# Optimization experiments

Hardware: AMD Instinct MI355X
Metric: run time of the kernel (lower is better)

The kernel has to match this reference:

```python
import jax, jax.numpy as jnp
import numpy as np

B, S, D_IN, D_OUT, RANK = 4, 2048, 4096, 4096, 16
SCALING = 32.0 / RANK  # alpha / rank
MASK_DENSITY = 0.01


def setup_inputs() -> dict:
    key = jax.random.key(0)
    ks = jax.random.split(key, 7)
    x = jax.random.normal(ks[0], (B, S, D_IN), dtype=jnp.float32)
    W = jax.random.normal(ks[1], (D_OUT, D_IN), dtype=jnp.float32) / np.sqrt(D_IN)
    b = jax.random.normal(ks[2], (D_OUT,), dtype=jnp.float32) * 0.01
    lora_A = jax.random.normal(ks[3], (RANK, D_IN), dtype=jnp.float32) / np.sqrt(D_IN)
    lora_B = jax.random.normal(ks[4], (D_OUT, RANK), dtype=jnp.float32) * 0.01
    delta = jax.random.normal(ks[5], (D_OUT, D_IN), dtype=jnp.float32) * 0.01
    mask = jax.random.bernoulli(ks[6], MASK_DENSITY, (D_OUT, D_IN))
    return {"x": x, "W": W, "b": b, "lora_A": lora_A, "lora_B": lora_B,
            "delta": delta, "mask": mask}


def reference(x, W, b, lora_A, lora_B, delta, mask):
    # frozen linear: [B,S,D_in] @ [D_in,D_out] + b
    out = jnp.einsum("bsd,od->bso", x, W) + b
    # LoRA branch: (x @ A^T) @ B^T * scaling
    out = out + jnp.einsum("bsr,or->bso", jnp.einsum("bsd,rd->bsr", x, lora_A), lora_B) * SCALING
    # sparse delta branch: F.linear(x, delta * mask)
    masked_delta = delta * mask.astype(delta.dtype)
    out = out + jnp.einsum("bsd,od->bso", x, masked_delta)
    return out
```

## Files before the change

kernel.cpp:

```cpp
#include <hip/hip_runtime.h>
#include <hip/hip_bf16.h>

typedef __hip_bfloat16 bf16;
typedef __attribute__((ext_vector_type(8))) short bf16x8;
typedef __attribute__((ext_vector_type(4))) float f32x4;
typedef __attribute__((ext_vector_type(4))) int int4v;

#define AS1 __attribute__((address_space(1)))
#define AS3 __attribute__((address_space(3)))

#define MDIM 8192
#define NDIM 4096
#define KDIM 4096
#define SCALING 2.0f

__global__ __launch_bounds__(256) void fold_weff(
    const float* __restrict__ W, const float* __restrict__ lA,
    const float* __restrict__ lB, const float* __restrict__ delta,
    const int* __restrict__ mask, bf16* __restrict__ Weff)
{
    int idx = blockIdx.x * 256 + threadIdx.x;
    int o   = idx >> 9;
    int d0  = (idx & 511) << 3;
    size_t base = (size_t)o * KDIM + d0;

    float Bo[16];
#pragma unroll
    for (int r = 0; r < 16; ++r) Bo[r] = lB[o * 16 + r];

    f32x4 wa = *(const f32x4*)(W + base);
    f32x4 wb = *(const f32x4*)(W + base + 4);
    f32x4 da = *(const f32x4*)(delta + base);
    f32x4 db = *(const f32x4*)(delta + base + 4);

    int mk[8];
    *(int4v*)(mk)     = *(const int4v*)(mask + base);
    *(int4v*)(mk + 4) = *(const int4v*)(mask + base + 4);

    float lor[8] = {0.f, 0.f, 0.f, 0.f, 0.f, 0.f, 0.f, 0.f};
#pragma unroll
    for (int r = 0; r < 16; ++r) {
        f32x4 aa = *(const f32x4*)(lA + (size_t)r * KDIM + d0);
        f32x4 ab = *(const f32x4*)(lA + (size_t)r * KDIM + d0 + 4);
#pragma unroll
        for (int e = 0; e < 4; ++e) {
            lor[e]     += Bo[r] * aa[e];
            lor[e + 4] += Bo[r] * ab[e];
        }
    }

    int4v ov4;
    bf16* ov = (bf16*)&ov4;
#pragma unroll
    for (int e = 0; e < 8; ++e) {
        float w = (e < 4) ? wa[e] : wb[e - 4];
        float d = (e < 4) ? da[e] : db[e - 4];
        float a = w + SCALING * lor[e];
        if (mk[e]) a += d;
        ov[e] = __float2bfloat16(a);
    }
    *(int4v*)(Weff + base) = ov4;
}

__global__ __launch_bounds__(256) void convert_x(
    const float* __restrict__ X, bf16* __restrict__ Xb)
{
    size_t i = ((size_t)blockIdx.x * 256 + threadIdx.x) * 8;
    f32x4 a = *(const f32x4*)(X + i);
    f32x4 b = *(const f32x4*)(X + i + 4);
    int4v ov4;
    bf16* ov = (bf16*)&ov4;
#pragma unroll
    for (int e = 0; e < 4; ++e) {
        ov[e]     = __float2bfloat16(a[e]);
        ov[e + 4] = __float2bfloat16(b[e]);
    }
    *(int4v*)(Xb + i) = ov4;
}

__global__ __launch_bounds__(256, 4) void gemm_bf16(
    const bf16* __restrict__ X, const bf16* __restrict__ Wt,
    const float* __restrict__ bias, float* __restrict__ out)
{
    __shared__ bf16 As[128 * 64];
    __shared__ bf16 Bs[128 * 64];

    const int tid  = threadIdx.x;
    const int lane = tid & 63;
    const int wave = tid >> 6;
    const int wm   = wave & 1;
    const int wn   = wave >> 1;
    const int quad = lane >> 4;
    const int l16  = lane & 15;

    const int bn = blockIdx.x * 128;
    const int bm = blockIdx.y * 128;
    const int cwave = tid & ~63;

    f32x4 acc[4][4];
#pragma unroll
    for (int i = 0; i < 4; ++i)
#pragma unroll
        for (int j = 0; j < 4; ++j)
            acc[i][j] = (f32x4){0.f, 0.f, 0.f, 0.f};

    for (int kt = 0; kt < KDIM / 64; ++kt) {
        const int k0 = kt * 64;
        if (kt) __syncthreads();
#pragma unroll
        for (int j = 0; j < 4; ++j) {
            const int c  = j * 256 + tid;
            const int m  = c >> 3;
            const int kc = (c & 7) ^ (m & 7);
            const int cb = j * 256 + cwave;
            __builtin_amdgcn_global_load_lds(
                (const AS1 void*)(X + (size_t)(bm + m) * KDIM + k0 + kc * 8),
                (AS3 void*)(As + cb * 8), 16, 0, 0);
            __builtin_amdgcn_global_load_lds(
                (const AS1 void*)(Wt + (size_t)(bn + m) * KDIM + k0 + kc * 8),
                (AS3 void*)(Bs + cb * 8), 16, 0, 0);
        }
        __syncthreads();

#pragma unroll
        for (int ks = 0; ks < 2; ++ks) {
            bf16x8 af[4], bfr[4];
#pragma unroll
            for (int i = 0; i < 4; ++i) {
                const int m   = wm * 64 + i * 16 + l16;
                const int kca = (ks * 4 + quad) ^ (m & 7);
                af[i] = *(const bf16x8*)(As + m * 64 + kca * 8);
                const int n   = wn * 64 + i * 16 + l16;
                const int kcb = (ks * 4 + quad) ^ (n & 7);
                bfr[i] = *(const bf16x8*)(Bs + n * 64 + kcb * 8);
            }
#pragma unroll
            for (int i = 0; i < 4; ++i)
#pragma unroll
                for (int j = 0; j < 4; ++j)
                    acc[i][j] = __builtin_amdgcn_mfma_f32_16x16x32_bf16(
                        af[i], bfr[j], acc[i][j], 0, 0, 0);
        }
    }

    float bv[4];
#pragma unroll
    for (int j = 0; j < 4; ++j)
        bv[j] = bias[bn + wn * 64 + j * 16 + l16];

#pragma unroll
    for (int i = 0; i < 4; ++i) {
        const int mg = bm + wm * 64 + i * 16 + quad * 4;
#pragma unroll
        for (int j = 0; j < 4; ++j) {
            const int ng = bn + wn * 64 + j * 16 + l16;
#pragma unroll
            for (int r = 0; r < 4; ++r)
                out[(size_t)(mg + r) * NDIM + ng] = acc[i][j][r] + bv[j];
        }
    }
}

__global__ __launch_bounds__(256, 3) void gemm_f32(
    const float* __restrict__ X, const bf16* __restrict__ Wt,
    const float* __restrict__ bias, float* __restrict__ out)
{
    __shared__ float Asf[128 * 64];
    __shared__ bf16  Bs[128 * 64];

    const int tid  = threadIdx.x;
    const int lane = tid & 63;
    const int wave = tid >> 6;
    const int wm   = wave & 1;
    const int wn   = wave >> 1;
    const int quad = lane >> 4;
    const int l16  = lane & 15;

    const int bn = blockIdx.x * 128;
    const int bm = blockIdx.y * 128;
    const int cwave = tid & ~63;

    f32x4 acc[4][4];
#pragma unroll
    for (int i = 0; i < 4; ++i)
#pragma unroll
        for (int j = 0; j < 4; ++j)
            acc[i][j] = (f32x4){0.f, 0.f, 0.f, 0.f};

    for (int kt = 0; kt < KDIM / 64; ++kt) {
        const int k0 = kt * 64;
        if (kt) __syncthreads();
#pragma unroll
        for (int j = 0; j < 8; ++j) {
            const int c  = j * 256 + tid;
            const int m  = c >> 4;
            const int kc = (c & 15) ^ (m & 15);
            const int cb = j * 256 + cwave;
            __builtin_amdgcn_global_load_lds(
                (const AS1 void*)(X + (size_t)(bm + m) * KDIM + k0 + kc * 4),
                (AS3 void*)(Asf + cb * 4), 16, 0, 0);
        }
#pragma unroll
        for (int j = 0; j < 4; ++j) {
            const int c  = j * 256 + tid;
            const int m  = c >> 3;
            const int kc = (c & 7) ^ (m & 7);
            const int cb = j * 256 + cwave;
            __builtin_amdgcn_global_load_lds(
                (const AS1 void*)(Wt + (size_t)(bn + m) * KDIM + k0 + kc * 8),
                (AS3 void*)(Bs + cb * 8), 16, 0, 0);
        }
        __syncthreads();

#pragma unroll
        for (int ks = 0; ks < 2; ++ks) {
            bf16x8 af[4], bfr[4];
#pragma unroll
            for (int i = 0; i < 4; ++i) {
                const int m  = wm * 64 + i * 16 + l16;
                const int k2 = (ks * 4 + quad) * 2;
                f32x4 lo = *(const f32x4*)(Asf + m * 64 + ((k2     ^ (m & 15)) * 4));
                f32x4 hi = *(const f32x4*)(Asf + m * 64 + (((k2+1) ^ (m & 15)) * 4));
                bf16 tmp[8];
#pragma unroll
                for (int e = 0; e < 4; ++e) {
                    tmp[e]     = __float2bfloat16(lo[e]);
                    tmp[e + 4] = __float2bfloat16(hi[e]);
                }
                af[i] = *(const bf16x8*)tmp;

                const int n   = wn * 64 + i * 16 + l16;
                const int kcb = (ks * 4 + quad) ^ (n & 7);
                bfr[i] = *(const bf16x8*)(Bs + n * 64 + kcb * 8);
            }
#pragma unroll
            for (int i = 0; i < 4; ++i)
#pragma unroll
                for (int j = 0; j < 4; ++j)
                    acc[i][j] = __builtin_amdgcn_mfma_f32_16x16x32_bf16(
                        af[i], bfr[j], acc[i][j], 0, 0, 0);
        }
    }

    float bv[4];
#pragma unroll
    for (int j = 0; j < 4; ++j)
        bv[j] = bias[bn + wn * 64 + j * 16 + l16];

#pragma unroll
    for (int i = 0; i < 4; ++i) {
        const int mg = bm + wm * 64 + i * 16 + quad * 4;
#pragma unroll
        for (int j = 0; j < 4; ++j) {
            const int ng = bn + wn * 64 + j * 16 + l16;
#pragma unroll
            for (int r = 0; r < 4; ++r)
                out[(size_t)(mg + r) * NDIM + ng] = acc[i][j][r] + bv[j];
        }
    }
}

extern "C" void kernel_launch(void* const* d_in, const int* in_sizes, int n_in,
                              void* d_out, int out_size, void* d_ws, size_t ws_size,
                              hipStream_t stream)
{
    const float* x     = (const float*)d_in[0];
    const float* W     = (const float*)d_in[1];
    const float* b     = (const float*)d_in[2];
    const float* lA    = (const float*)d_in[3];
    const float* lB    = (const float*)d_in[4];
    const float* delta = (const float*)d_in[5];
    const int*   mask  = (const int*)d_in[6];
    float* out = (float*)d_out;

    bf16* Weff = (bf16*)d_ws;
    bf16* Xb   = (bf16*)((char*)d_ws + (size_t)NDIM * KDIM * 2);

    const size_t need = (size_t)NDIM * KDIM * 2 + (size_t)MDIM * KDIM * 2;

    fold_weff<<<dim3((NDIM * KDIM / 8) / 256), 256, 0, stream>>>(
        W, lA, lB, delta, mask, Weff);

    if (ws_size >= need) {
        convert_x<<<dim3((MDIM * KDIM / 8) / 256), 256, 0, stream>>>(x, Xb);
        gemm_bf16<<<dim3(NDIM / 128, MDIM / 128), 256, 0, stream>>>(
            Xb, Weff, b, out);
    } else {
        gemm_f32<<<dim3(NDIM / 128, MDIM / 128), 256, 0, stream>>>(
            x, Weff, b, out);
    }
}
```

Before: 647.4 us.

## Switch GEMM to 32x32x16 MFMA and merge prep kernels into one launch

The bf16 GEMM now uses 32x32x16 bf16 MFMA tiles (a 2x2 grid of 32x32 accumulators per wave) in place of a 4x4 grid of 16x16x32 tiles. This halves the number of LDS fragment loads per MFMA and raises math density per instruction. The weight-fold and x-conversion kernels are fused into a single prep launch to save one launch and allow overlap. The fp32 fallback GEMM and the workspace-size check are removed, so the code now assumes the workspace is always large enough.

After: 677.5 us. +4.7%, slower.

```diff
diff --git a/kernel.cpp b/kernel.cpp
--- a/kernel.cpp
+++ b/kernel.cpp
@@ -4,6 +4,7 @@
 typedef __hip_bfloat16 bf16;
 typedef __attribute__((ext_vector_type(8))) short bf16x8;
 typedef __attribute__((ext_vector_type(4))) float f32x4;
+typedef __attribute__((ext_vector_type(16))) float f32x16;
 typedef __attribute__((ext_vector_type(4))) int int4v;
 
 #define AS1 __attribute__((address_space(1)))
@@ -14,68 +15,70 @@
 #define KDIM 4096
 #define SCALING 2.0f
 
-__global__ __launch_bounds__(256) void fold_weff(
+#define FOLD_BLOCKS (NDIM * KDIM / 8 / 256)
+#define CONV_BLOCKS (MDIM * KDIM / 8 / 256)
+
+__global__ __launch_bounds__(256) void prep(
     const float* __restrict__ W, const float* __restrict__ lA,
     const float* __restrict__ lB, const float* __restrict__ delta,
-    const int* __restrict__ mask, bf16* __restrict__ Weff)
+    const int* __restrict__ mask, const float* __restrict__ X,
+    bf16* __restrict__ Weff, bf16* __restrict__ Xb)
 {
-    int idx = blockIdx.x * 256 + threadIdx.x;
-    int o   = idx >> 9;
-    int d0  = (idx & 511) << 3;
-    size_t base = (size_t)o * KDIM + d0;
+    if (blockIdx.x < FOLD_BLOCKS) {
+        int idx = blockIdx.x * 256 + threadIdx.x;
+        int o   = idx >> 9;
+        int d0  = (idx & 511) << 3;
+        size_t base = (size_t)o * KDIM + d0;
 
-    float Bo[16];
+        float Bo[16];
 #pragma unroll
-    for (int r = 0; r < 16; ++r) Bo[r] = lB[o * 16 + r];
+        for (int r = 0; r < 16; ++r) Bo[r] = lB[o * 16 + r];
 
-    f32x4 wa = *(const f32x4*)(W + base);
-    f32x4 wb = *(const f32x4*)(W + base + 4);
-    f32x4 da = *(const f32x4*)(delta + base);
-    f32x4 db = *(const f32x4*)(delta + base + 4);
+        f32x4 wa = *(const f32x4*)(W + base);
+        f32x4 wb = *(const f32x4*)(W + base + 4);
+        f32x4 da = *(const f32x4*)(delta + base);
+        f32x4 db = *(const f32x4*)(delta + base + 4);
 
-    int mk[8];
-    *(int4v*)(mk)     = *(const int4v*)(mask + base);
-    *(int4v*)(mk + 4) = *(const int4v*)(mask + base + 4);
+        int mk[8];
+        *(int4v*)(mk)     = *(const int4v*)(mask + base);
+        *(int4v*)(mk + 4) = *(const int4v*)(mask + base + 4);
 
-    float lor[8] = {0.f, 0.f, 0.f, 0.f, 0.f, 0.f, 0.f, 0.f};
+        float lor[8] = {0.f, 0.f, 0.f, 0.f, 0.f, 0.f, 0.f, 0.f};
 #pragma unroll
-    for (int r = 0; r < 16; ++r) {
-        f32x4 aa = *(const f32x4*)(lA + (size_t)r * KDIM + d0);
-        f32x4 ab = *(const f32x4*)(lA + (size_t)r * KDIM + d0 + 4);
+        for (int r = 0; r < 16; ++r) {
+            f32x4 aa = *(const f32x4*)(lA + (size_t)r * KDIM + d0);
+            f32x4 ab = *(const f32x4*)(lA + (size_t)r * KDIM + d0 + 4);
+#pragma unroll
+            for (int e = 0; e < 4; ++e) {
+                lor[e]     += Bo[r] * aa[e];
+                lor[e + 4] += Bo[r] * ab[e];
+            }
+        }
+
+        int4v ov4;
+        bf16* ov = (bf16*)&ov4;
+#pragma unroll
+        for (int e = 0; e < 8; ++e) {
+            float w = (e < 4) ? wa[e] : wb[e - 4];
+            float d = (e < 4) ? da[e] : db[e - 4];
+            float a = w + SCALING * lor[e];
+            if (mk[e]) a += d;
+            ov[e] = __float2bfloat16(a);
+        }
+        *(int4v*)(Weff + base) = ov4;
+    } else {
+        size_t i = ((size_t)(blockIdx.x - FOLD_BLOCKS) * 256 + threadIdx.x) * 8;
+        f32x4 a = *(const f32x4*)(X + i);
+        f32x4 b = *(const f32x4*)(X + i + 4);
+        int4v ov4;
+        bf16* ov = (bf16*)&ov4;
 #pragma unroll
         for (int e = 0; e < 4; ++e) {
-            lor[e]     += Bo[r] * aa[e];
-            lor[e + 4] += Bo[r] * ab[e];
+            ov[e]     = __float2bfloat16(a[e]);
+            ov[e + 4] = __float2bfloat16(b[e]);
         }
+        *(int4v*)(Xb + i) = ov4;
     }
-
-    int4v ov4;
-    bf16* ov = (bf16*)&ov4;
-#pragma unroll
-    for (int e = 0; e < 8; ++e) {
-        float w = (e < 4) ? wa[e] : wb[e - 4];
-        float d = (e < 4) ? da[e] : db[e - 4];
-        float a = w + SCALING * lor[e];
-        if (mk[e]) a += d;
-        ov[e] = __float2bfloat16(a);
-    }
-    *(int4v*)(Weff + base) = ov4;
-}
-
-__global__ __launch_bounds__(256) void convert_x(
-    const float* __restrict__ X, bf16* __restrict__ Xb)
-{
-    size_t i = ((size_t)blockIdx.x * 256 + threadIdx.x) * 8;
-    f32x4 a = *(const f32x4*)(X + i);
-    f32x4 b = *(const f32x4*)(X + i + 4);
-    int4v ov4;
-    bf16* ov = (bf16*)&ov4;
-#pragma unroll
-    for (int e = 0; e < 4; ++e) {
-        ov[e]     = __float2bfloat16(a[e]);
-        ov[e + 4] = __float2bfloat16(b[e]);
-    }
-    *(int4v*)(Xb + i) = ov4;
 }
 
 __global__ __launch_bounds__(256, 4) void gemm_bf16(
@@ -90,19 +93,21 @@
     const int wave = tid >> 6;
     const int wm   = wave & 1;
     const int wn   = wave >> 1;
-    const int quad = lane >> 4;
-    const int l16  = lane & 15;
+    const int half = lane >> 5;
+    const int l32  = lane & 31;
 
     const int bn = blockIdx.x * 128;
     const int bm = blockIdx.y * 128;
     const int cwave = tid & ~63;
 
-    f32x4 acc[4][4];
+    f32x16 acc[2][2];
 #pragma unroll
-    for (int i = 0; i < 4; ++i)
+    for (int i = 0; i < 2; ++i)
 #pragma unroll
-        for (int j = 0; j < 4; ++j)
-            acc[i][j] = (f32x4){0.f, 0.f, 0.f, 0.f};
+        for (int j = 0; j < 2; ++j)
+#pragma unroll
+            for (int r = 0; r < 16; ++r)
+                acc[i][j][r] = 0.f;
 
     for (int kt = 0; kt < KDIM / 64; ++kt) {
         const int k0 = kt * 64;
@@ -123,139 +128,43 @@
         __syncthreads();
 
 #pragma unroll
-        for (int ks = 0; ks < 2; ++ks) {
-            bf16x8 af[4], bfr[4];
+        for (int ks = 0; ks < 4; ++ks) {
+            const int kcl = ks * 2 + half;
+            bf16x8 af[2], bfr[2];
 #pragma unroll
-            for (int i = 0; i < 4; ++i) {
-                const int m   = wm * 64 + i * 16 + l16;
-                const int kca = (ks * 4 + quad) ^ (m & 7);
-                af[i] = *(const bf16x8*)(As + m * 64 + kca * 8);
-                const int n   = wn * 64 + i * 16 + l16;
-                const int kcb = (ks * 4 + quad) ^ (n & 7);
-                bfr[i] = *(const bf16x8*)(Bs + n * 64 + kcb * 8);
+            for (int i = 0; i < 2; ++i) {
+                const int m = wm * 64 + i * 32 + l32;
+                af[i]  = *(const bf16x8*)(As + m * 64 + (kcl ^ (m & 7)) * 8);
+                const int n = wn * 64 + i * 32 + l32;
+                bfr[i] = *(const bf16x8*)(Bs + n * 64 + (kcl ^ (n & 7)) * 8);
             }
 #pragma unroll
-            for (int i = 0; i < 4; ++i)
+            for (int i = 0; i < 2; ++i)
 #pragma unroll
-                for (int j = 0; j < 4; ++j)
-                    acc[i][j] = __builtin_amdgcn_mfma_f32_16x16x32_bf16(
+                for (int j = 0; j < 2; ++j)
+                    acc[i][j] = __builtin_amdgcn_mfma_f32_32x32x16_bf16(
                         af[i], bfr[j], acc[i][j], 0, 0, 0);
         }
     }
 
-    float bv[4];
+    float bv[2];
 #pragma unroll
-    for (int j = 0; j < 4; ++j)
-        bv[j] = bias[bn + wn * 64 + j * 16 + l16];
+    for (int j = 0; j < 2; ++j)
+        bv[j] = bias[bn + wn * 64 + j * 32 + l32];
 
 #pragma unroll
-    for (int i = 0; i < 4; ++i) {
-        const int mg = bm + wm * 64 + i * 16 + quad * 4;
+    for (int i = 0; i < 2; ++i) {
 #pragma unroll
-        for (int j = 0; j < 4; ++j) {
-            const int ng = bn + wn * 64 + j * 16 + l16;
+        for (int j = 0; j < 2; ++j) {
+            const int ng = bn + wn * 64 + j * 32 + l32;
 #pragma unroll
-            for (int r = 0; r < 4; ++r)
-                out[(size_t)(mg + r) * NDIM + ng] = acc[i][j][r] + bv[j];
-        }
-    }
-}
-
-__global__ __launch_bounds__(256, 3) void gemm_f32(
-    const float* __restrict__ X, const bf16* __restrict__ Wt,
-    const float* __restrict__ bias, float* __restrict__ out)
-{
-    __shared__ float Asf[128 * 64];
-    __shared__ bf16  Bs[128 * 64];
-
-    const int tid  = threadIdx.x;
-    const int lane = tid & 63;
-    const int wave = tid >> 6;
-    const int wm   = wave & 1;
-    const int wn   = wave >> 1;
-    const int quad = lane >> 4;
-    const int l16  = lane & 15;
-
-    const int bn = blockIdx.x * 128;
-    const int bm = blockIdx.y * 128;
-    const int cwave = tid & ~63;
-
-    f32x4 acc[4][4];
+            for (int g = 0; g < 4; ++g) {
 #pragma unroll
-    for (int i = 0; i < 4; ++i)
-#pragma unroll
-        for (int j = 0; j < 4; ++j)
-            acc[i][j] = (f32x4){0.f, 0.f, 0.f, 0.f};
-
-    for (int kt = 0; kt < KDIM / 64; ++kt) {
-        const int k0 = kt * 64;
-        if (kt) __syncthreads();
-#pragma unroll
-        for (int j = 0; j < 8; ++j) {
-            const int c  = j * 256 + tid;
-            const int m  = c >> 4;
-            const int kc = (c & 15) ^ (m & 15);
-            const int cb = j * 256 + cwave;
-            __builtin_amdgcn_global_load_lds(
-                (const AS1 void*)(X + (size_t)(bm + m) * KDIM + k0 + kc * 4),
-                (AS3 void*)(Asf + cb * 4), 16, 0, 0);
-        }
-#pragma unroll
-        for (int j = 0; j < 4; ++j) {
-            const int c  = j * 256 + tid;
-            const int m  = c >> 3;
-            const int kc = (c & 7) ^ (m & 7);
-            const int cb = j * 256 + cwave;
-            __builtin_amdgcn_global_load_lds(
-                (const AS1 void*)(Wt + (size_t)(bn + m) * KDIM + k0 + kc * 8),
-                (AS3 void*)(Bs + cb * 8), 16, 0, 0);
-        }
-        __syncthreads();
-
-#pragma unroll
-        for (int ks = 0; ks < 2; ++ks) {
-            bf16x8 af[4], bfr[4];
-#pragma unroll
-            for (int i = 0; i < 4; ++i) {
-                const int m  = wm * 64 + i * 16 + l16;
-                const int k2 = (ks * 4 + quad) * 2;
-                f32x4 lo = *(const f32x4*)(Asf + m * 64 + ((k2     ^ (m & 15)) * 4));
-                f32x4 hi = *(const f32x4*)(Asf + m * 64 + (((k2+1) ^ (m & 15)) * 4));
-                bf16 tmp[8];
-#pragma unroll
-                for (int e = 0; e < 4; ++e) {
-                    tmp[e]     = __float2bfloat16(lo[e]);
-                    tmp[e + 4] = __float2bfloat16(hi[e]);
+                for (int r = 0; r < 4; ++r) {
+                    const int mg = bm + wm * 64 + i * 32 + r + 8 * g + 4 * half;
+                    out[(size_t)mg * NDIM + ng] = acc[i][j][4 * g + r] + bv[j];
                 }
-                af[i] = *(const bf16x8*)tmp;
-
-                const int n   = wn * 64 + i * 16 + l16;
-                const int kcb = (ks * 4 + quad) ^ (n & 7);
-                bfr[i] = *(const bf16x8*)(Bs + n * 64 + kcb * 8);
             }
-#pragma unroll
-            for (int i = 0; i < 4; ++i)
-#pragma unroll
-                for (int j = 0; j < 4; ++j)
-                    acc[i][j] = __builtin_amdgcn_mfma_f32_16x16x32_bf16(
-                        af[i], bfr[j], acc[i][j], 0, 0, 0);
-        }
-    }
-
-    float bv[4];
-#pragma unroll
-    for (int j = 0; j < 4; ++j)
-        bv[j] = bias[bn + wn * 64 + j * 16 + l16];
-
-#pragma unroll
-    for (int i = 0; i < 4; ++i) {
-        const int mg = bm + wm * 64 + i * 16 + quad * 4;
-#pragma unroll
-        for (int j = 0; j < 4; ++j) {
-            const int ng = bn + wn * 64 + j * 16 + l16;
-#pragma unroll
-            for (int r = 0; r < 4; ++r)
-                out[(size_t)(mg + r) * NDIM + ng] = acc[i][j][r] + bv[j];
         }
     }
 }
@@ -276,17 +185,9 @@
     bf16* Weff = (bf16*)d_ws;
     bf16* Xb   = (bf16*)((char*)d_ws + (size_t)NDIM * KDIM * 2);
 
-    const size_t need = (size_t)NDIM * KDIM * 2 + (size_t)MDIM * KDIM * 2;
+    prep<<<dim3(FOLD_BLOCKS + CONV_BLOCKS), 256, 0, stream>>>(
+        W, lA, lB, delta, mask, x, Weff, Xb);
 
-    fold_weff<<<dim3((NDIM * KDIM / 8) / 256), 256, 0, stream>>>(
-        W, lA, lB, delta, mask, Weff);
-
-    if (ws_size >= need) {
-        convert_x<<<dim3((MDIM * KDIM / 8) / 256), 256, 0, stream>>>(x, Xb);
-        gemm_bf16<<<dim3(NDIM / 128, MDIM / 128), 256, 0, stream>>>(
-            Xb, Weff, b, out);
-    } else {
-        gemm_f32<<<dim3(NDIM / 128, MDIM / 128), 256, 0, stream>>>(
-            x, Weff, b, out);
-    }
+    gemm_bf16<<<dim3(NDIM / 128, MDIM / 128), 256, 0, stream>>>(
+        Xb, Weff, b, out);
 }
```
